# Performance work log

Measured on AMD Instinct MI355X. Metric: run time of the kernel, lower is better.

Reference implementation:

```python
import jax, jax.numpy as jnp
import numpy as np

N = 50000
E = 800000
IN_C = 256
H1 = 64
H2 = 64
OUT_C = 32
HEADS = 7
NEG_SLOPE = 0.2


def _gat_layer(x, src, dst, W, a_src, a_dst, b, heads, ch, n_nodes):
    # x: [N, F_in]; W: [F_in, heads*ch]; a_src/a_dst: [heads, ch]; b: [heads*ch]
    h = (x @ W).reshape(n_nodes, heads, ch)                      # [N, H, C]
    alpha_s = jnp.einsum('nhc,hc->nh', h, a_src)                 # [N, H]
    alpha_d = jnp.einsum('nhc,hc->nh', h, a_dst)                 # [N, H]
    e = jax.nn.leaky_relu(alpha_s[src] + alpha_d[dst], NEG_SLOPE)  # [E, H]
    # segment softmax grouped by destination node
    m = jax.ops.segment_max(e, dst, num_segments=n_nodes)        # [N, H]
    e = jnp.exp(e - m[dst])
    denom = jax.ops.segment_sum(e, dst, num_segments=n_nodes)    # [N, H]
    alpha = e / (denom[dst] + 1e-16)                             # [E, H]
    msg = h[src] * alpha[:, :, None]                             # [E, H, C]
    out = jax.ops.segment_sum(msg, dst, num_segments=n_nodes)    # [N, H, C]
    return out.reshape(n_nodes, heads * ch) + b


def setup_inputs() -> dict:
    key = jax.random.key(0)
    ks = jax.random.split(key, 16)
    x = jax.random.normal(ks[0], (N, IN_C), dtype=jnp.float32)
    edge_index = jax.random.randint(ks[1], (2, E), 0, N, dtype=jnp.int32)

    def glorot(k, shape):
        fan = shape[0] + shape[-1]
        return jax.random.normal(k, shape, dtype=jnp.float32) * jnp.sqrt(2.0 / fan)

    W1 = glorot(ks[2], (IN_C, HEADS * H1))
    a1_src = glorot(ks[3], (HEADS, H1))
    a1_dst = glorot(ks[4], (HEADS, H1))
    b1 = jnp.zeros((HEADS * H1,), jnp.float32)

    W2 = glorot(ks[5], (HEADS * H1, HEADS * H2))
    a2_src = glorot(ks[6], (HEADS, H2))
    a2_dst = glorot(ks[7], (HEADS, H2))
    b2 = jnp.zeros((HEADS * H2,), jnp.float32)

    W3 = glorot(ks[8], (HEADS * H2, 1 * OUT_C))
    a3_src = glorot(ks[9], (1, OUT_C))
    a3_dst = glorot(ks[10], (1, OUT_C))
    b3 = jnp.zeros((OUT_C,), jnp.float32)

    return {"x": x, "edge_index": edge_index,
            "W1": W1, "a1_src": a1_src, "a1_dst": a1_dst, "b1": b1,
            "W2": W2, "a2_src": a2_src, "a2_dst": a2_dst, "b2": b2,
            "W3": W3, "a3_src": a3_src, "a3_dst": a3_dst, "b3": b3}


def reference(x, edge_index, W1, a1_src, a1_dst, b1, W2, a2_src, a2_dst, b2,
              W3, a3_src, a3_dst, b3):
    # PyG GATConv adds self-loops by default
    loops = jnp.arange(N, dtype=edge_index.dtype)
    src = jnp.concatenate([edge_index[0], loops])
    dst = jnp.concatenate([edge_index[1], loops])
    # dropout is identity in eval mode
    h = _gat_layer(x, src, dst, W1, a1_src, a1_dst, b1, HEADS, H1, N)
    h = jax.nn.relu(h)
    h = _gat_layer(h, src, dst, W2, a2_src, a2_dst, b2, HEADS, H2, N)
    h = jax.nn.relu(h)
    h = _gat_layer(h, src, dst, W3, a3_src, a3_dst, b3, 1, OUT_C, N)
    return jax.nn.log_softmax(h, axis=1)
```

## Files before the change

kernel.cpp:

```cpp
#include <hip/hip_runtime.h>
#include <hip/hip_bf16.h>
#include <hip/hip_fp16.h>

#define NN 50000
#define NP 50176
#define EE 800000
#define ET (EE + NN)

typedef __attribute__((ext_vector_type(4))) float f32x4;

static __device__ __forceinline__ float bf2f(__hip_bfloat16 x) { return __bfloat162float(x); }
static __device__ __forceinline__ ushort f2bu(float f) {
    union { __hip_bfloat16 b; ushort u; } c;
    c.b = __float2bfloat16(f);
    return c.u;
}
static __device__ __forceinline__ unsigned char f2fp8(float v) {
    int p = __builtin_amdgcn_cvt_pk_fp8_f32(v, v, 0, false);
    return (unsigned char)(p & 0xff);
}
static __device__ __forceinline__ unsigned pk4fp8(float a, float b, float c, float d) {
    unsigned lo = (unsigned)__builtin_amdgcn_cvt_pk_fp8_f32(a, b, 0, false) & 0xffffu;
    unsigned hi = (unsigned)__builtin_amdgcn_cvt_pk_fp8_f32(c, d, 0, false) & 0xffffu;
    return lo | (hi << 16);
}
static __device__ __forceinline__ void fp8acc4(unsigned v, float w, float* acc) {
#if __has_builtin(__builtin_amdgcn_cvt_pk_f32_fp8)
    auto f01 = __builtin_amdgcn_cvt_pk_f32_fp8((int)v, false);
    auto f23 = __builtin_amdgcn_cvt_pk_f32_fp8((int)v, true);
    acc[0] += w * f01[0];
    acc[1] += w * f01[1];
    acc[2] += w * f23[0];
    acc[3] += w * f23[1];
#else
    acc[0] += w * __builtin_amdgcn_cvt_f32_fp8(v, 0);
    acc[1] += w * __builtin_amdgcn_cvt_f32_fp8(v, 1);
    acc[2] += w * __builtin_amdgcn_cvt_f32_fp8(v, 2);
    acc[3] += w * __builtin_amdgcn_cvt_f32_fp8(v, 3);
#endif
}
static __device__ __forceinline__ void gl2lds(const unsigned char* g, unsigned char* l) {
    __builtin_amdgcn_global_load_lds(
        (const __attribute__((address_space(1))) void*)g,
        (__attribute__((address_space(3))) void*)l,
        16, 0, 0);
}

#define PA1 (256 * 448)
#define PA2 (448 * 448)
#define PA3 (448 * 32)
#define PXQ (NN * 64)
#define PTOT (PA1 + PA2 + PA3 + PXQ)
#define PBLK ((PTOT + 255) / 256)
#define CBLK ((ET + 255) / 256)

__global__ void gat_prepcnt_kernel(const float* __restrict__ W1, const float* __restrict__ W2,
                                   const float* __restrict__ W3, const float* __restrict__ x,
                                   unsigned char* __restrict__ Wt1, unsigned char* __restrict__ Wt2,
                                   unsigned char* __restrict__ Wt3, unsigned char* __restrict__ xb,
                                   const int* __restrict__ ei, int* __restrict__ cnt) {
    int b = blockIdx.x;
    if (b >= PBLK) {
        int i = (b - PBLK) * 256 + threadIdx.x;
        if (i < ET) {
            int dst = (i < EE) ? ei[EE + i] : (i - EE);
            atomicAdd(&cnt[dst], 1);
        }
        return;
    }
    int i = b * 256 + threadIdx.x;
    if (i < PA1) {
        int k = i / 448, n = i - k * 448;
        Wt1[(size_t)n * 256 + k] = f2fp8(W1[i]);
        return;
    }
    i -= PA1;
    if (i < PA2) {
        int k = i / 448, n = i - k * 448;
        Wt2[(size_t)n * 448 + k] = f2fp8(W2[i]);
        return;
    }
    i -= PA2;
    if (i < PA3) {
        int k = i / 32, n = i - k * 32;
        Wt3[(size_t)n * 448 + k] = f2fp8(W3[i]);
        return;
    }
    i -= PA3;
    if (i < PXQ) {
        float4 f = ((const float4*)x)[i];
        ((unsigned*)xb)[i] = pk4fp8(f.x, f.y, f.z, f.w);
    }
}

__global__ void gat_scanall_kernel(const int* __restrict__ cnt, int* __restrict__ row_ptr) {
    __shared__ int sm[1024];
    const int C = 49;
    int t = threadIdx.x;
    int base = t * C;
    int s = 0;
    for (int i = 0; i < C; i++) {
        int idx = base + i;
        if (idx < NN) s += cnt[idx];
    }
    sm[t] = s;
    __syncthreads();
    for (int o = 1; o < 1024; o <<= 1) {
        int v = (t >= o) ? sm[t - o] : 0;
        __syncthreads();
        sm[t] += v;
        __syncthreads();
    }
    int run = (t > 0) ? sm[t - 1] : 0;
    for (int i = 0; i < C; i++) {
        int idx = base + i;
        if (idx < NN) {
            run += cnt[idx];
            row_ptr[idx + 1] = run;
        }
    }
    if (t == 0) row_ptr[0] = 0;
}

__global__ void gat_fill_kernel(const int* __restrict__ ei, const int* __restrict__ row_ptr,
                                int* __restrict__ fillc, int* __restrict__ colA) {
    int i = blockIdx.x * blockDim.x + threadIdx.x;
    if (i >= ET) return;
    int s, d;
    if (i < EE) { s = ei[i]; d = ei[EE + i]; }
    else        { s = d = i - EE; }
    int pos = row_ptr[d] + atomicAdd(&fillc[d], 1);
    colA[pos] = s;
}

#define GBN 64
#define GBK 64

template <int RF, int DOA, int OM>
__global__ __launch_bounds__(256) void gat_gemm_kernel(
    const unsigned char* __restrict__ A, const unsigned char* __restrict__ Wt,
    void* __restrict__ Cv,
    const float* __restrict__ Asrc, const float* __restrict__ Adst,
    float* __restrict__ as8, float* __restrict__ ad8,
    int M, int K, int N) {
    constexpr int GBM = RF * 64;
    __shared__ __align__(16) unsigned char As[2][GBM * GBK];
    __shared__ __align__(16) unsigned char Bs[2][GBN * GBK];
    int tid = threadIdx.x;
    int wave = tid >> 6, lane = tid & 63;
    int lrow = lane & 15, lq = lane >> 4;
    int m0 = blockIdx.x * GBM, n0 = blockIdx.y * GBN;
    int srow = lane >> 2, schunk = (lane & 3) * 16;
    f32x4 acc[RF][4] = {};

    int KT = K / GBK;
    {
#pragma unroll
        for (int q = 0; q < RF; q++) {
            const unsigned char* gp = A + (size_t)(m0 + wave * RF * 16 + q * 16 + srow) * K + schunk;
            gl2lds(gp, &As[0][(wave * RF * 16 + q * 16) * GBK]);
        }
        const unsigned char* gb = Wt + (size_t)(n0 + wave * 16 + srow) * K + schunk;
        gl2lds(gb, &Bs[0][wave * 16 * GBK]);
    }
    for (int kt = 0; kt < KT; kt++) {
        __syncthreads();
        if (kt + 1 < KT) {
            int nb = (kt + 1) & 1, k0 = (kt + 1) * GBK;
#pragma unroll
            for (int q = 0; q < RF; q++) {
                const unsigned char* gp = A + (size_t)(m0 + wave * RF * 16 + q * 16 + srow) * K + k0 + schunk;
                gl2lds(gp, &As[nb][(wave * RF * 16 + q * 16) * GBK]);
            }
            const unsigned char* gb = Wt + (size_t)(n0 + wave * 16 + srow) * K + k0 + schunk;
            gl2lds(gb, &Bs[nb][wave * 16 * GBK]);
        }
        int b = kt & 1;
#pragma unroll
        for (int s = 0; s < 2; s++) {
            long af[RF];
#pragma unroll
            for (int rf = 0; rf < RF; rf++)
                af[rf] = *(const long*)&As[b][(wave * RF * 16 + rf * 16 + lrow) * GBK + s * 32 + lq * 8];
#pragma unroll
            for (int ng = 0; ng < 4; ng++) {
                long bf = *(const long*)&Bs[b][(ng * 16 + lrow) * GBK + s * 32 + lq * 8];
#pragma unroll
                for (int rf = 0; rf < RF; rf++)
                    acc[rf][ng] = __builtin_amdgcn_mfma_f32_16x16x32_fp8_fp8(af[rf], bf, acc[rf][ng], 0, 0, 0);
            }
        }
    }
#pragma unroll
    for (int rf = 0; rf < RF; rf++)
#pragma unroll
        for (int ng = 0; ng < 4; ng++)
#pragma unroll
            for (int r = 0; r < 4; r++) {
                int row = m0 + wave * RF * 16 + rf * 16 + lq * 4 + r;
                int colI = n0 + ng * 16 + lrow;
                if (row < M && colI < N) {
                    if constexpr (OM == 0)
                        ((__hip_bfloat16*)Cv)[(size_t)row * N + colI] = __float2bfloat16(acc[rf][ng][r]);
                    else
                        ((unsigned char*)Cv)[(size_t)row * N + colI] = f2fp8(acc[rf][ng][r]);
                }
            }
    if constexpr (DOA == 1) {
        int head = blockIdx.y;
        float as_l[4], ad_l[4];
#pragma unroll
        for (int ng = 0; ng < 4; ng++) {
            as_l[ng] = Asrc[head * 64 + ng * 16 + lrow];
            ad_l[ng] = Adst[head * 64 + ng * 16 + lrow];
        }
#pragma unroll
        for (int rf = 0; rf < RF; rf++)
#pragma unroll
            for (int r = 0; r < 4; r++) {
                float ps = 0.f, pd = 0.f;
#pragma unroll
                for (int ng = 0; ng < 4; ng++) {
                    ps += acc[rf][ng][r] * as_l[ng];
                    pd += acc[rf][ng][r] * ad_l[ng];
                }
#pragma unroll
                for (int o = 1; o < 16; o <<= 1) {
                    ps += __shfl_xor(ps, o);
                    pd += __shfl_xor(pd, o);
                }
                int row = m0 + wave * RF * 16 + rf * 16 + lq * 4 + r;
                if (lrow == 0 && row < M) {
                    as8[(size_t)row * 8 + head] = ps;
                    ad8[(size_t)row * 8 + head] = pd;
                }
            }
    } else if constexpr (DOA == 2) {
        float as_l[2], ad_l[2];
#pragma unroll
        for (int ng = 0; ng < 2; ng++) {
            as_l[ng] = Asrc[ng * 16 + lrow];
            ad_l[ng] = Adst[ng * 16 + lrow];
        }
#pragma unroll
        for (int rf = 0; rf < RF; rf++)
#pragma unroll
            for (int r = 0; r < 4; r++) {
                float ps = acc[rf][0][r] * as_l[0] + acc[rf][1][r] * as_l[1];
                float pd = acc[rf][0][r] * ad_l[0] + acc[rf][1][r] * ad_l[1];
#pragma unroll
                for (int o = 1; o < 16; o <<= 1) {
                    ps += __shfl_xor(ps, o);
                    pd += __shfl_xor(pd, o);
                }
                int row = m0 + wave * RF * 16 + rf * 16 + lq * 4 + r;
                if (lrow == 0 && row < M) {
                    as8[(size_t)row * 8] = ps;
                    ad8[(size_t)row * 8] = pd;
                }
            }
    }
}

__global__ void gat_aggC7_kernel(const int* __restrict__ rp, const int* __restrict__ colA,
                                 const float* __restrict__ as8, const float* __restrict__ ad8,
                                 const unsigned char* __restrict__ h8,
                                 const float* __restrict__ bias,
                                 unsigned char* __restrict__ outp) {
    int d = blockIdx.x * 4 + (threadIdx.x >> 6);
    if (d >= NN) return;
    int lane = threadIdx.x & 63;
    if (lane >= 56) return;
    int hh = lane >> 3;
    float adh = ad8[(size_t)d * 8 + hh];
    int s0 = rp[d], s1 = rp[d + 1];
    float acc[8] = {0.f, 0.f, 0.f, 0.f, 0.f, 0.f, 0.f, 0.f};
    float den = 0.f;
    int j = s0;
    for (; j + 4 <= s1; j += 4) {
        int sA = colA[j], sB = colA[j + 1], sC = colA[j + 2], sD = colA[j + 3];
        float eA = as8[(size_t)sA * 8 + hh] + adh;
        float eB = as8[(size_t)sB * 8 + hh] + adh;
        float eC = as8[(size_t)sC * 8 + hh] + adh;
        float eD = as8[(size_t)sD * 8 + hh] + adh;
        uint2 hA = *(const uint2*)(h8 + (size_t)sA * 448 + lane * 8);
        uint2 hB = *(const uint2*)(h8 + (size_t)sB * 448 + lane * 8);
        uint2 hC = *(const uint2*)(h8 + (size_t)sC * 448 + lane * 8);
        uint2 hD = *(const uint2*)(h8 + (size_t)sD * 448 + lane * 8);
        eA = (eA > 0.f) ? eA : 0.2f * eA;
        eB = (eB > 0.f) ? eB : 0.2f * eB;
        eC = (eC > 0.f) ? eC : 0.2f * eC;
        eD = (eD > 0.f) ? eD : 0.2f * eD;
        float wA = __expf(eA), wB = __expf(eB);
        float wC = __expf(eC), wD = __expf(eD);
        den += (wA + wB) + (wC + wD);
        fp8acc4(hA.x, wA, &acc[0]); fp8acc4(hA.y, wA, &acc[4]);
        fp8acc4(hB.x, wB, &acc[0]); fp8acc4(hB.y, wB, &acc[4]);
        fp8acc4(hC.x, wC, &acc[0]); fp8acc4(hC.y, wC, &acc[4]);
        fp8acc4(hD.x, wD, &acc[0]); fp8acc4(hD.y, wD, &acc[4]);
    }
    for (; j < s1; j++) {
        int s = colA[j];
        float e = as8[(size_t)s * 8 + hh] + adh;
        e = (e > 0.f) ? e : 0.2f * e;
        float w = __expf(e);
        uint2 hv = *(const uint2*)(h8 + (size_t)s * 448 + lane * 8);
        den += w;
        fp8acc4(hv.x, w, &acc[0]);
        fp8acc4(hv.y, w, &acc[4]);
    }
    float inv = 1.f / (den + 1e-16f);
    const float4* bp = (const float4*)(bias + lane * 8);
    float4 bb0 = bp[0], bb1 = bp[1];
    float bv[8] = {bb0.x, bb0.y, bb0.z, bb0.w, bb1.x, bb1.y, bb1.z, bb1.w};
    float o[8];
#pragma unroll
    for (int k = 0; k < 8; k++) o[k] = fmaxf(acc[k] * inv + bv[k], 0.f);
    uint2 packed;
    packed.x = pk4fp8(o[0], o[1], o[2], o[3]);
    packed.y = pk4fp8(o[4], o[5], o[6], o[7]);
    *(uint2*)(outp + (size_t)d * 448 + lane * 8) = packed;
}

__global__ void gat_aggCF_kernel(const int* __restrict__ rp, const int* __restrict__ colA,
                                 const float* __restrict__ as8, const float* __restrict__ ad8,
                                 const __hip_bfloat16* __restrict__ h,
                                 const float* __restrict__ bias,
                                 float* __restrict__ outp) {
    int wid = blockIdx.x * 4 + (threadIdx.x >> 6);
    int lane = threadIdx.x & 63;
    int half = lane >> 5, c = lane & 31;
    int dreal = wid * 2 + half;
    bool valid = dreal < NN;
    int d = valid ? dreal : (NN - 1);
    float adh = ad8[(size_t)d * 8];
    int s0 = rp[d], s1 = rp[d + 1];
    float acc = 0.f, den = 0.f;
    int j = s0;
    for (; j + 2 <= s1; j += 2) {
        int sA = colA[j], sB = colA[j + 1];
        float eA = as8[(size_t)sA * 8] + adh;
        float eB = as8[(size_t)sB * 8] + adh;
        float vA = bf2f(h[(size_t)sA * 32 + c]);
        float vB = bf2f(h[(size_t)sB * 32 + c]);
        eA = (eA > 0.f) ? eA : 0.2f * eA;
        eB = (eB > 0.f) ? eB : 0.2f * eB;
        float wA = __expf(eA), wB = __expf(eB);
        den += wA + wB;
        acc += wA * vA + wB * vB;
    }
    for (; j < s1; j++) {
        int s = colA[j];
        float e = as8[(size_t)s * 8] + adh;
        e = (e > 0.f) ? e : 0.2f * e;
        float w = __expf(e);
        den += w;
        acc += w * bf2f(h[(size_t)s * 32 + c]);
    }
    float o = acc / (den + 1e-16f) + bias[c];
    float t = o;
#pragma unroll
    for (int off = 16; off > 0; off >>= 1) t = fmaxf(t, __shfl_xor(t, off));
    float ex = __expf(o - t);
#pragma unroll
    for (int off = 16; off > 0; off >>= 1) ex += __shfl_xor(ex, off);
    float res = o - t - __logf(ex);
    if (valid) outp[(size_t)d * 32 + c] = res;
}

extern "C" void kernel_launch(void* const* d_in, const int* in_sizes, int n_in,
                              void* d_out, int out_size, void* d_ws, size_t ws_size,
                              hipStream_t stream) {
    const float* x   = (const float*)d_in[0];
    const int*   ei  = (const int*)d_in[1];
    const float* W1  = (const float*)d_in[2];
    const float* a1s = (const float*)d_in[3];
    const float* a1d = (const float*)d_in[4];
    const float* b1  = (const float*)d_in[5];
    const float* W2  = (const float*)d_in[6];
    const float* a2s = (const float*)d_in[7];
    const float* a2d = (const float*)d_in[8];
    const float* b2  = (const float*)d_in[9];
    const float* W3  = (const float*)d_in[10];
    const float* a3s = (const float*)d_in[11];
    const float* a3d = (const float*)d_in[12];
    const float* b3  = (const float*)d_in[13];
    float* out = (float*)d_out;

    char* w = (char*)d_ws;
    unsigned char* hbuf8 = (unsigned char*)w;
    __hip_bfloat16* hbuf3 = (__hip_bfloat16*)w;
    unsigned char* xb  = (unsigned char*)(w + (size_t)NP * 448);
    unsigned char* act = xb + (size_t)NP * 256;
    float* as8 = (float*)(act + (size_t)NP * 448);
    float* ad8 = as8 + (size_t)NN * 8;
    int* cnt     = (int*)(ad8 + (size_t)NN * 8);
    int* fillc   = cnt + NN;
    int* row_ptr = fillc + NN;
    int* colA    = row_ptr + (NN + 4);
    char* pw = (char*)(colA + ET);
    pw = (char*)(((uintptr_t)pw + 15) & ~(uintptr_t)15);
    unsigned char* Wt1 = (unsigned char*)pw;
    unsigned char* Wt2 = Wt1 + 448 * 256;
    unsigned char* Wt3 = Wt2 + 448 * 448;

    hipMemsetAsync(cnt, 0, 2 * (size_t)NN * sizeof(int), stream);

    gat_prepcnt_kernel<<<PBLK + CBLK, 256, 0, stream>>>(W1, W2, W3, x, Wt1, Wt2, Wt3, xb, ei, cnt);
    gat_scanall_kernel<<<1, 1024, 0, stream>>>(cnt, row_ptr);
    gat_fill_kernel<<<CBLK, 256, 0, stream>>>(ei, row_ptr, fillc, colA);

    dim3 gemmBlk(256);
    int mtiles = NP / 256;
    int mtiles1 = NP / 64;
    int aggBlocks = (NN + 3) / 4;

    gat_gemm_kernel<4, 1, 1><<<dim3(mtiles, 7), gemmBlk, 0, stream>>>(
        xb, Wt1, hbuf8, a1s, a1d, as8, ad8, NN, 256, 448);
    gat_aggC7_kernel<<<aggBlocks, 256, 0, stream>>>(row_ptr, colA, as8, ad8, hbuf8, b1, act);

    gat_gemm_kernel<4, 1, 1><<<dim3(mtiles, 7), gemmBlk, 0, stream>>>(
        act, Wt2, hbuf8, a2s, a2d, as8, ad8, NN, 448, 448);
    gat_aggC7_kernel<<<aggBlocks, 256, 0, stream>>>(row_ptr, colA, as8, ad8, hbuf8, b2, act);

    gat_gemm_kernel<1, 2, 0><<<dim3(mtiles1, 1), gemmBlk, 0, stream>>>(
        act, Wt3, hbuf3, a3s, a3d, as8, ad8, NN, 448, 32);
    int fBlocks = (NN + 7) / 8;
    gat_aggCF_kernel<<<fBlocks, 256, 0, stream>>>(row_ptr, colA, as8, ad8, hbuf3, b3, out);
}
```

Before: 572.9 us.

## Replace single-block prefix scan with three-pass multi-block scan

The CSR row-pointer scan used to run in one 1024-thread block where each thread serially walked 49 strided counts. It is now a three-kernel scan: per-block scans, a scan of the 196 block totals, and an add-back of offsets. This spreads the work across many CUs with coalesced access, at the cost of two extra kernel launches and an intermediate buffer.

```diff
diff --git a/kernel.cpp b/kernel.cpp
--- a/kernel.cpp
+++ b/kernel.cpp
@@ -6,6 +6,7 @@
 #define NP 50176
 #define EE 800000
 #define ET (EE + NN)
+#define NB_SCAN ((NN + 255) / 256)
 
 typedef __attribute__((ext_vector_type(4))) float f32x4;
 
@@ -93,33 +94,45 @@
     }
 }
 
-__global__ void gat_scanall_kernel(const int* __restrict__ cnt, int* __restrict__ row_ptr) {
-    __shared__ int sm[1024];
-    const int C = 49;
-    int t = threadIdx.x;
-    int base = t * C;
-    int s = 0;
-    for (int i = 0; i < C; i++) {
-        int idx = base + i;
-        if (idx < NN) s += cnt[idx];
-    }
-    sm[t] = s;
+__global__ void gat_scan1_kernel(const int* __restrict__ cnt, int* __restrict__ tmp,
+                                 int* __restrict__ part) {
+    __shared__ int sm[256];
+    int tid = threadIdx.x;
+    int i = blockIdx.x * 256 + tid;
+    int v = (i < NN) ? cnt[i] : 0;
+    sm[tid] = v;
     __syncthreads();
-    for (int o = 1; o < 1024; o <<= 1) {
-        int v = (t >= o) ? sm[t - o] : 0;
+    for (int o = 1; o < 256; o <<= 1) {
+        int t = (tid >= o) ? sm[tid - o] : 0;
         __syncthreads();
-        sm[t] += v;
+        sm[tid] += t;
         __syncthreads();
     }
-    int run = (t > 0) ? sm[t - 1] : 0;
-    for (int i = 0; i < C; i++) {
-        int idx = base + i;
-        if (idx < NN) {
-            run += cnt[idx];
-            row_ptr[idx + 1] = run;
-        }
-    }
-    if (t == 0) row_ptr[0] = 0;
+    if (i < NN) tmp[i] = sm[tid];
+    if (tid == 255) part[blockIdx.x] = sm[255];
+}
+
+__global__ void gat_scan2_kernel(int* __restrict__ part) {
+    __shared__ int sm[256];
+    int tid = threadIdx.x;
+    int v = (tid < NB_SCAN) ? part[tid] : 0;
+    sm[tid] = v;
+    __syncthreads();
+    for (int o = 1; o < 256; o <<= 1) {
+        int t = (tid >= o) ? sm[tid - o] : 0;
+        __syncthreads();
+        sm[tid] += t;
+        __syncthreads();
+    }
+    part[tid] = sm[tid];
+}
+
+__global__ void gat_scan3_kernel(const int* __restrict__ tmp, const int* __restrict__ part,
+                                 int* __restrict__ row_ptr) {
+    int i = blockIdx.x * 256 + threadIdx.x;
+    int off = (blockIdx.x > 0) ? part[blockIdx.x - 1] : 0;
+    if (i < NN) row_ptr[i + 1] = tmp[i] + off;
+    if (i == 0) row_ptr[0] = 0;
 }
 
 __global__ void gat_fill_kernel(const int* __restrict__ ei, const int* __restrict__ row_ptr,
@@ -397,7 +410,9 @@
     int* cnt     = (int*)(ad8 + (size_t)NN * 8);
     int* fillc   = cnt + NN;
     int* row_ptr = fillc + NN;
-    int* colA    = row_ptr + (NN + 4);
+    int* tmp     = row_ptr + (NN + 4);
+    int* part    = tmp + NN;
+    int* colA    = part + 256;
     char* pw = (char*)(colA + ET);
     pw = (char*)(((uintptr_t)pw + 15) & ~(uintptr_t)15);
     unsigned char* Wt1 = (unsigned char*)pw;
@@ -407,7 +422,9 @@
     hipMemsetAsync(cnt, 0, 2 * (size_t)NN * sizeof(int), stream);
 
     gat_prepcnt_kernel<<<PBLK + CBLK, 256, 0, stream>>>(W1, W2, W3, x, Wt1, Wt2, Wt3, xb, ei, cnt);
-    gat_scanall_kernel<<<1, 1024, 0, stream>>>(cnt, row_ptr);
+    gat_scan1_kernel<<<NB_SCAN, 256, 0, stream>>>(cnt, tmp, part);
+    gat_scan2_kernel<<<1, 256, 0, stream>>>(part);
+    gat_scan3_kernel<<<NB_SCAN, 256, 0, stream>>>(tmp, part, row_ptr);
     gat_fill_kernel<<<CBLK, 256, 0, stream>>>(ei, row_ptr, fillc, colA);
 
     dim3 gemmBlk(256);
```

Measured after the change: 494.1 us. -13.8%, faster.
